# Kernel tuning notes

Measured on AMD Instinct MI355X. Metric: run time of the kernel, lower is better.

The kernel has to match this reference:

```python
import jax, jax.numpy as jnp
import numpy as np

N_NODES = 100000
N_EDGES = 2500000
N_GRAPHS = 1024


def setup_inputs() -> dict:
    key = jax.random.key(0)
    ks = jax.random.split(key, 12)
    inp = {
        "x": jax.random.normal(ks[0], (N_NODES, 7), dtype=jnp.float32),
        "e": jax.random.uniform(ks[1], (N_EDGES,), dtype=jnp.float32),
        "W1": jax.random.normal(ks[2], (7, 32), dtype=jnp.float32) * 0.3,
        "b1": jnp.zeros((32,), dtype=jnp.float32),
        "W2": jax.random.normal(ks[3], (32, 32), dtype=jnp.float32) * 0.2,
        "b2": jnp.zeros((32,), dtype=jnp.float32),
        "W3": jax.random.normal(ks[4], (32, 32), dtype=jnp.float32) * 0.2,
        "b3": jnp.zeros((32,), dtype=jnp.float32),
        "W4": jax.random.normal(ks[5], (32, 2), dtype=jnp.float32) * 0.2,
        "b4": jnp.zeros((2,), dtype=jnp.float32),
        "src": jax.random.randint(ks[6], (N_EDGES,), 0, N_NODES, dtype=jnp.int32),
        "dst": jax.random.randint(ks[7], (N_EDGES,), 0, N_NODES, dtype=jnp.int32),
        "graph_id": jnp.sort(jax.random.randint(ks[8], (N_NODES,), 0, N_GRAPHS, dtype=jnp.int32)),
        "n_graphs": N_GRAPHS,
    }
    return inp


def _graph_conv(feat, W, b, src, dst, norm_out, norm_in, edge_weight=None):
    # DGL GraphConv, norm='both': D_out^{-1/2} -> (weighted) sum aggregation -> D_in^{-1/2} -> linear
    n = feat.shape[0]
    h = feat * norm_out[:, None]
    m = h[src]  # [E, d] gather
    if edge_weight is not None:
        m = m * edge_weight[:, None]
    agg = jax.ops.segment_sum(m, dst, num_segments=n)  # [N, d]
    agg = agg * norm_in[:, None]
    return agg @ W + b


def reference(x, e, W1, b1, W2, b2, W3, b3, W4, b4, src, dst, graph_id, n_graphs):
    n = x.shape[0]
    ones_e = jnp.ones((src.shape[0],), dtype=x.dtype)
    deg_out = jax.ops.segment_sum(ones_e, src, num_segments=n)
    deg_in = jax.ops.segment_sum(ones_e, dst, num_segments=n)
    norm_out = jax.lax.rsqrt(jnp.clip(deg_out, 1.0))  # degs.clamp(min=1)^{-1/2}
    norm_in = jax.lax.rsqrt(jnp.clip(deg_in, 1.0))

    h = jax.nn.relu(_graph_conv(x, W1, b1, src, dst, norm_out, norm_in, edge_weight=e))
    h = jax.nn.relu(_graph_conv(h, W2, b2, src, dst, norm_out, norm_in))
    h = jax.nn.relu(_graph_conv(h, W3, b3, src, dst, norm_out, norm_in))
    h = _graph_conv(h, W4, b4, src, dst, norm_out, norm_in)

    # dgl.mean_nodes: per-graph mean of node features
    sums = jax.ops.segment_sum(h, graph_id, num_segments=n_graphs)  # [G, 2]
    cnts = jax.ops.segment_sum(jnp.ones((n,), dtype=h.dtype), graph_id, num_segments=n_graphs)
    return sums / jnp.clip(cnts, 1.0)[:, None]
```

## Files before the change

### kernel.cpp

```cpp
#include <hip/hip_runtime.h>

#define NN 100000
#define NE 2500000
#define BK_SHIFT 7
#define BK_NODES 128
#define NBUCK ((NN + BK_NODES - 1) / BK_NODES)
#define TILE 4096
#define NTILES ((NE + TILE - 1) / TILE)
#define SRC_MASK 0x1FFFF


__global__ __launch_bounds__(256) void k_tilecnt2(const int* __restrict__ src,
                                                  const int* __restrict__ dst,
                                                  int* __restrict__ tot_d, int* __restrict__ tot_s,
                                                  int E) {
    __shared__ int cd[NBUCK];
    __shared__ int cs[NBUCK];
    int base = blockIdx.x * TILE;
    for (int i = threadIdx.x; i < NBUCK; i += 256) { cd[i] = 0; cs[i] = 0; }
    __syncthreads();
#pragma unroll
    for (int k = 0; k < 16; ++k) {
        int idx = base + threadIdx.x + k * 256;
        if (idx < E) {
            atomicAdd(&cd[dst[idx] >> BK_SHIFT], 1);
            atomicAdd(&cs[src[idx] >> BK_SHIFT], 1);
        }
    }
    __syncthreads();
    for (int i = threadIdx.x; i < NBUCK; i += 256) {
        int c = cd[i]; if (c) atomicAdd(&tot_d[i], c);
        c = cs[i];     if (c) atomicAdd(&tot_s[i], c);
    }
}

__global__ __launch_bounds__(1024) void k_bucket_scan(const int* __restrict__ tot_d,
                                                      const int* __restrict__ tot_s,
                                                      int* __restrict__ base_d, int* __restrict__ base_s,
                                                      int* __restrict__ cursor_d, int* __restrict__ cursor_s,
                                                      int* __restrict__ row_ptr, int E) {
    __shared__ int sh[1024];
    int tid = threadIdx.x;
    int v = (tid < NBUCK) ? tot_d[tid] : 0;
    sh[tid] = v;
    __syncthreads();
#pragma unroll
    for (int off = 1; off < 1024; off <<= 1) {
        int t = (tid >= off) ? sh[tid - off] : 0;
        __syncthreads();
        sh[tid] += t;
        __syncthreads();
    }
    if (tid < NBUCK) { int ex = sh[tid] - v; base_d[tid] = ex; cursor_d[tid] = ex; }
    if (tid == 0) { base_d[NBUCK] = E; row_ptr[NN] = E; }
    __syncthreads();
    v = (tid < NBUCK) ? tot_s[tid] : 0;
    sh[tid] = v;
    __syncthreads();
#pragma unroll
    for (int off = 1; off < 1024; off <<= 1) {
        int t = (tid >= off) ? sh[tid - off] : 0;
        __syncthreads();
        sh[tid] += t;
        __syncthreads();
    }
    if (tid < NBUCK) { int ex = sh[tid] - v; base_s[tid] = ex; cursor_s[tid] = ex; }
    if (tid == 0) base_s[NBUCK] = E;
}

__global__ __launch_bounds__(256) void k_binpass2(
    const int* __restrict__ src, const int* __restrict__ dst, const float* __restrict__ ew,
    int* __restrict__ cursor_d, int* __restrict__ cursor_s,
    int2* __restrict__ stage2, unsigned char* __restrict__ stage_s, int E) {
    __shared__ int cnt_d[NBUCK];
    __shared__ int gpos_d[NBUCK];
    __shared__ int cnt_s[NBUCK];
    __shared__ int gpos_s[NBUCK];

    int base = blockIdx.x * TILE;
    for (int i = threadIdx.x; i < NBUCK; i += 256) { cnt_d[i] = 0; cnt_s[i] = 0; }
    __syncthreads();

    int w0[16]; float w1[16]; int pd[16]; int rs[16];
#pragma unroll
    for (int k = 0; k < 16; ++k) {
        int idx = base + threadIdx.x + k * 256;
        pd[k] = -1;
        if (idx < E) {
            int s = src[idx], d = dst[idx];
            w1[k] = ew[idx];
            int bd = d >> BK_SHIFT;
            w0[k] = s | ((d & (BK_NODES - 1)) << 17);
            int rd = atomicAdd(&cnt_d[bd], 1);
            pd[k] = bd | (rd << 10);
            rs[k] = atomicAdd(&cnt_s[s >> BK_SHIFT], 1);
        }
    }
    __syncthreads();

    for (int i = threadIdx.x; i < NBUCK; i += 256) {
        int c = cnt_d[i]; if (c) gpos_d[i] = atomicAdd(&cursor_d[i], c);
        c = cnt_s[i];     if (c) gpos_s[i] = atomicAdd(&cursor_s[i], c);
    }
    __syncthreads();

#pragma unroll
    for (int k = 0; k < 16; ++k) {
        if (pd[k] >= 0) {
            int bd = pd[k] & 1023, rd = pd[k] >> 10;
            stage2[gpos_d[bd] + rd] = make_int2(w0[k], __float_as_int(w1[k]));
            int s = w0[k] & SRC_MASK;
            stage_s[gpos_s[s >> BK_SHIFT] + rs[k]] = (unsigned char)(s & (BK_NODES - 1));
        }
    }
}

__global__ __launch_bounds__(256) void k_prep_src(
    const int* __restrict__ base_s, const unsigned char* __restrict__ stage_s, const float* __restrict__ x,
    float* __restrict__ no, float* __restrict__ xs, int N) {
    __shared__ int cnt[BK_NODES];
    int b = blockIdx.x;
    int beg = base_s[b], end = base_s[b + 1];
    if (threadIdx.x < BK_NODES) cnt[threadIdx.x] = 0;
    __syncthreads();
    for (int j = beg + threadIdx.x; j < end; j += 256) atomicAdd(&cnt[stage_s[j]], 1);
    __syncthreads();
    if (threadIdx.x < BK_NODES) {
        int n = (b << BK_SHIFT) + threadIdx.x;
        if (n < N) {
            float nov = rsqrtf(fmaxf((float)cnt[threadIdx.x], 1.0f));
            no[n] = nov;
#pragma unroll
            for (int f = 0; f < 7; ++f) xs[n * 8 + f] = x[n * 7 + f] * nov;
            xs[n * 8 + 7] = 0.f;
        }
    }
}

__global__ __launch_bounds__(256) void k_scatter2(
    const int* __restrict__ base_d, const int2* __restrict__ stage2,
    int* __restrict__ row_ptr, float* __restrict__ ni,
    int* __restrict__ csr_src, float* __restrict__ csr_w, int N) {
    __shared__ int cnt[BK_NODES];
    __shared__ int scn[BK_NODES];
    __shared__ int cur[BK_NODES];
    int b = blockIdx.x;
    int beg = base_d[b], end = base_d[b + 1];
    if (threadIdx.x < BK_NODES) cnt[threadIdx.x] = 0;
    __syncthreads();
    for (int j = beg + threadIdx.x; j < end; j += 256) atomicAdd(&cnt[stage2[j].x >> 17], 1);
    __syncthreads();
    int v = (threadIdx.x < BK_NODES) ? cnt[threadIdx.x] : 0;
    if (threadIdx.x < BK_NODES) scn[threadIdx.x] = v;
    __syncthreads();
#pragma unroll
    for (int off = 1; off < BK_NODES; off <<= 1) {
        int t = (threadIdx.x < BK_NODES && threadIdx.x >= off) ? scn[threadIdx.x - off] : 0;
        __syncthreads();
        if (threadIdx.x < BK_NODES) scn[threadIdx.x] += t;
        __syncthreads();
    }
    if (threadIdx.x < BK_NODES) {
        int ex = scn[threadIdx.x] - v;
        cur[threadIdx.x] = beg + ex;
        int n = (b << BK_SHIFT) + threadIdx.x;
        if (n < N) {
            row_ptr[n] = beg + ex;
            ni[n] = rsqrtf(fmaxf((float)v, 1.0f));
        }
    }
    __syncthreads();
    for (int j = beg + threadIdx.x; j < end; j += 256) {
        int2 t = stage2[j];
        int dl = t.x >> 17;
        int pos = atomicAdd(&cur[dl], 1);
        csr_src[pos] = t.x & SRC_MASK;
        csr_w[pos] = __int_as_float(t.y);
    }
}


__global__ __launch_bounds__(256) void k_layer1(
    const int* __restrict__ rp, const int* __restrict__ csr_src, const float* __restrict__ csr_w,
    const float* __restrict__ xs, const float* __restrict__ ni, const float* __restrict__ no,
    const float* __restrict__ W1, const float* __restrict__ b1, float* __restrict__ h1c, int N) {
    __shared__ float sW[7 * 32];
    __shared__ float sb[32];
    __shared__ float sh7[32][8];
    for (int i = threadIdx.x; i < 7 * 32; i += 256) sW[i] = W1[i];
    if (threadIdx.x < 32) sb[threadIdx.x] = b1[threadIdx.x];

    int g = threadIdx.x >> 3, lane = threadIdx.x & 7;
    int node = blockIdx.x * 32 + g;
    float acc = 0.f;
    if (node < N) {
        int beg = rp[node], end = rp[node + 1];
        for (int j0 = beg; j0 < end; j0 += 8) {
            int ms = 0; float mw = 0.f;
            if (j0 + lane < end) {
                ms = csr_src[j0 + lane];
                mw = csr_w[j0 + lane];
            }
            int m = end - j0; if (m > 8) m = 8;
            float a0 = 0.f, a1 = 0.f, a2 = 0.f, a3 = 0.f;
            int k = 0;
            for (; k + 4 <= m; k += 4) {
                int s0 = __shfl(ms, k, 8);     float w0 = __shfl(mw, k, 8);
                int s1 = __shfl(ms, k + 1, 8); float w1 = __shfl(mw, k + 1, 8);
                int s2 = __shfl(ms, k + 2, 8); float w2 = __shfl(mw, k + 2, 8);
                int s3 = __shfl(ms, k + 3, 8); float w3 = __shfl(mw, k + 3, 8);
                a0 += xs[s0 * 8 + lane] * w0;
                a1 += xs[s1 * 8 + lane] * w1;
                a2 += xs[s2 * 8 + lane] * w2;
                a3 += xs[s3 * 8 + lane] * w3;
            }
            for (; k < m; ++k) {
                int s = __shfl(ms, k, 8);
                float w = __shfl(mw, k, 8);
                a0 += xs[s * 8 + lane] * w;
            }
            acc += (a0 + a1) + (a2 + a3);
        }
        acc *= ni[node];
    }
    sh7[g][lane] = acc;
    __syncthreads();

    int g2 = threadIdx.x >> 5, l32 = threadIdx.x & 31;
#pragma unroll
    for (int t = 0; t < 4; ++t) {
        int nl = t * 8 + g2;
        int node2 = blockIdx.x * 32 + nl;
        if (node2 < N) {
            float o = sb[l32];
#pragma unroll
            for (int k = 0; k < 7; ++k) o += sh7[nl][k] * sW[k * 32 + l32];
            h1c[(size_t)(l32 >> 3) * N * 8 + (size_t)node2 * 8 + (l32 & 7)] =
                fmaxf(o, 0.f) * no[node2];
        }
    }
}

__device__ __forceinline__ void proc8(int msr, int mm, const float* __restrict__ tbl, int lane,
                                      float& a0, float& a1, float& a2, float& a3) {
    if (mm >= 8) {
        a0 += tbl[__shfl(msr, 0, 8) * 8 + lane];
        a1 += tbl[__shfl(msr, 1, 8) * 8 + lane];
        a2 += tbl[__shfl(msr, 2, 8) * 8 + lane];
        a3 += tbl[__shfl(msr, 3, 8) * 8 + lane];
        a0 += tbl[__shfl(msr, 4, 8) * 8 + lane];
        a1 += tbl[__shfl(msr, 5, 8) * 8 + lane];
        a2 += tbl[__shfl(msr, 6, 8) * 8 + lane];
        a3 += tbl[__shfl(msr, 7, 8) * 8 + lane];
    } else {
        int kl = 0;
        for (; kl + 4 <= mm; kl += 4) {
            a0 += tbl[__shfl(msr, kl, 8) * 8 + lane];
            a1 += tbl[__shfl(msr, kl + 1, 8) * 8 + lane];
            a2 += tbl[__shfl(msr, kl + 2, 8) * 8 + lane];
            a3 += tbl[__shfl(msr, kl + 3, 8) * 8 + lane];
        }
        for (; kl < mm; ++kl) a0 += tbl[__shfl(msr, kl, 8) * 8 + lane];
    }
}

__global__ __launch_bounds__(256) void k_aggc(
    const int* __restrict__ rp, const int* __restrict__ csr_src, const float* __restrict__ hc_in,
    const float* __restrict__ ni, float* __restrict__ aggout, int N) {
    int g = threadIdx.x >> 3, lane = threadIdx.x & 7;
    int c = blockIdx.y;
    int node = blockIdx.x * 32 + g;
    if (node >= N) return;
    const float* tbl = hc_in + (size_t)c * N * 8;
    int beg = rp[node], end = rp[node + 1];
    float acc = 0.f;
    for (int j0 = beg; j0 < end; j0 += 32) {
        int m = end - j0; if (m > 32) m = 32;
        int ms0 = (j0 + lane < end) ? csr_src[j0 + lane] : 0;
        int ms1 = (j0 + 8 + lane < end) ? csr_src[j0 + 8 + lane] : 0;
        int ms2 = (j0 + 16 + lane < end) ? csr_src[j0 + 16 + lane] : 0;
        int ms3 = (j0 + 24 + lane < end) ? csr_src[j0 + 24 + lane] : 0;
        float a0 = 0.f, a1 = 0.f, a2 = 0.f, a3 = 0.f;
        proc8(ms0, m, tbl, lane, a0, a1, a2, a3);
        if (m > 8)  proc8(ms1, m - 8, tbl, lane, a0, a1, a2, a3);
        if (m > 16) proc8(ms2, m - 16, tbl, lane, a0, a1, a2, a3);
        if (m > 24) proc8(ms3, m - 24, tbl, lane, a0, a1, a2, a3);
        acc += (a0 + a1) + (a2 + a3);
    }
    acc *= ni[node];
    aggout[(size_t)c * N * 8 + (size_t)node * 8 + lane] = acc;
}

__global__ __launch_bounds__(256) void k_mm2(
    const float* __restrict__ agg, const float* __restrict__ W, const float* __restrict__ bia,
    const float* __restrict__ no, float* __restrict__ hc_out, int N) {
    __shared__ float sW[32 * 32];
    __shared__ float sb[32];
    __shared__ float shv[8][32];
    for (int i = threadIdx.x; i < 1024; i += 256) sW[i] = W[i];
    if (threadIdx.x < 32) sb[threadIdx.x] = bia[threadIdx.x];
    int g = threadIdx.x >> 5, lane = threadIdx.x & 31;
    int n = blockIdx.x * 8 + g;
    if (n < N)
        shv[g][lane] = agg[(size_t)(lane >> 3) * N * 8 + (size_t)n * 8 + (lane & 7)];
    __syncthreads();
    if (n < N) {
        float o = sb[lane];
#pragma unroll
        for (int k = 0; k < 32; ++k) o += shv[g][k] * sW[k * 32 + lane];
        hc_out[(size_t)(lane >> 3) * N * 8 + (size_t)n * 8 + (lane & 7)] =
            fmaxf(o, 0.f) * no[n];
    }
}

__global__ __launch_bounds__(256) void k_mm3(
    const float* __restrict__ agg, const float* __restrict__ W3, const float* __restrict__ b3,
    const float* __restrict__ W4, const float* __restrict__ no, float2* __restrict__ h4pre, int N) {
    __shared__ float sW[32 * 32];
    __shared__ float sb[32];
    __shared__ float sW4[64];
    __shared__ float shv[8][32];
    for (int i = threadIdx.x; i < 1024; i += 256) sW[i] = W3[i];
    if (threadIdx.x < 32) sb[threadIdx.x] = b3[threadIdx.x];
    if (threadIdx.x < 64) sW4[threadIdx.x] = W4[threadIdx.x];
    int g = threadIdx.x >> 5, lane = threadIdx.x & 31;
    int n = blockIdx.x * 8 + g;
    if (n < N)
        shv[g][lane] = agg[(size_t)(lane >> 3) * N * 8 + (size_t)n * 8 + (lane & 7)];
    __syncthreads();
    if (n < N) {
        float o = sb[lane];
#pragma unroll
        for (int k = 0; k < 32; ++k) o += shv[g][k] * sW[k * 32 + lane];
        float t = fmaxf(o, 0.f) * no[n];
        float px = t * sW4[lane * 2 + 0];
        float py = t * sW4[lane * 2 + 1];
#pragma unroll
        for (int off = 16; off; off >>= 1) {
            px += __shfl_xor(px, off, 32);
            py += __shfl_xor(py, off, 32);
        }
        if (lane == 0) h4pre[n] = make_float2(px, py);
    }
}

__global__ void k_agg4(const int* __restrict__ rp, const int* __restrict__ csr_src,
                       const float2* __restrict__ h4pre, const float* __restrict__ ni,
                       float2* __restrict__ agg2, int N) {
    int n = blockIdx.x * blockDim.x + threadIdx.x;
    if (n >= N) return;
    int beg = rp[n], end = rp[n + 1];
    float ax0 = 0.f, ay0 = 0.f, ax1 = 0.f, ay1 = 0.f;
    int j = beg;
    for (; j + 2 <= end; j += 2) {
        int s0 = csr_src[j], s1 = csr_src[j + 1];
        float2 v0 = h4pre[s0];
        float2 v1 = h4pre[s1];
        ax0 += v0.x; ay0 += v0.y;
        ax1 += v1.x; ay1 += v1.y;
    }
    if (j < end) {
        float2 v = h4pre[csr_src[j]];
        ax0 += v.x; ay0 += v.y;
    }
    float w = ni[n];
    agg2[n] = make_float2((ax0 + ax1) * w, (ay0 + ay1) * w);
}

__global__ void k_pool(const float2* __restrict__ agg2, const int* __restrict__ gid,
                       const float* __restrict__ b4, float* __restrict__ out, int N) {
    int g = blockIdx.x;
    int lo = 0, hi = N;
    while (lo < hi) { int m = (lo + hi) >> 1; if (gid[m] < g) lo = m + 1; else hi = m; }
    int start = lo;
    int lo2 = start, hi2 = N;
    while (lo2 < hi2) { int m = (lo2 + hi2) >> 1; if (gid[m] < g + 1) lo2 = m + 1; else hi2 = m; }
    int end = lo2;
    float sx = 0.f, sy = 0.f;
    for (int n = start + threadIdx.x; n < end; n += 64) {
        float2 v = agg2[n];
        sx += v.x;
        sy += v.y;
    }
#pragma unroll
    for (int off = 32; off; off >>= 1) {
        sx += __shfl_down(sx, off, 64);
        sy += __shfl_down(sy, off, 64);
    }
    if (threadIdx.x == 0) {
        int cnt = end - start;
        float inv = 1.0f / fmaxf((float)cnt, 1.0f);
        float scale = (float)cnt * inv;
        out[g * 2 + 0] = sx * inv + b4[0] * scale;
        out[g * 2 + 1] = sy * inv + b4[1] * scale;
    }
}


extern "C" void kernel_launch(void* const* d_in, const int* in_sizes, int n_in,
                              void* d_out, int out_size, void* d_ws, size_t ws_size,
                              hipStream_t stream) {
    const float* x   = (const float*)d_in[0];
    const float* e   = (const float*)d_in[1];
    const float* W1  = (const float*)d_in[2];
    const float* b1  = (const float*)d_in[3];
    const float* W2  = (const float*)d_in[4];
    const float* b2  = (const float*)d_in[5];
    const float* W3  = (const float*)d_in[6];
    const float* b3  = (const float*)d_in[7];
    const float* W4  = (const float*)d_in[8];
    const float* b4  = (const float*)d_in[9];
    const int*   src = (const int*)d_in[10];
    const int*   dst = (const int*)d_in[11];
    const int*   gid = (const int*)d_in[12];
    float* out = (float*)d_out;

    const int N = NN, E = NE;
    const int G = out_size / 2;

    int* ws_i = (int*)d_ws;
    int* tot_d    = ws_i;
    int* tot_s    = ws_i + 1024;
    int* base_d   = ws_i + 2048;
    int* base_s   = ws_i + 3072;
    int* cursor_d = ws_i + 4096;
    int* cursor_s = ws_i + 5120;
    int* row_ptr  = ws_i + 6144;
    int* csr_src  = ws_i + 6144 + (size_t)N + 4;
    float* csr_w  = (float*)(ws_i + 6144 + (size_t)N + 4 + (size_t)E);
    unsigned char* stage_s = (unsigned char*)csr_w;

    float* fbase = (float*)(ws_i + 6144 + (size_t)N + 4 + 2 * (size_t)E);
    float* no_b  = fbase;
    float* ni_b  = fbase + (size_t)N;
    float* xs    = fbase + (size_t)2 * N;
    float* h1c   = fbase + (size_t)10 * N;
    float* h2c   = fbase + (size_t)42 * N;
    float2* h4pre = (float2*)(fbase + (size_t)74 * N);
    float2* agg2  = (float2*)(fbase + (size_t)76 * N);
    int2* stage2 = (int2*)(fbase + (size_t)10 * N);
    float* agg3 = h1c;

    hipMemsetAsync(ws_i, 0, 2048 * sizeof(int), stream);

    k_tilecnt2<<<NTILES, 256, 0, stream>>>(src, dst, tot_d, tot_s, E);
    k_bucket_scan<<<1, 1024, 0, stream>>>(tot_d, tot_s, base_d, base_s, cursor_d, cursor_s, row_ptr, E);
    k_binpass2<<<NTILES, 256, 0, stream>>>(src, dst, e, cursor_d, cursor_s, stage2, stage_s, E);
    k_prep_src<<<NBUCK, 256, 0, stream>>>(base_s, stage_s, x, no_b, xs, N);
    k_scatter2<<<NBUCK, 256, 0, stream>>>(base_d, stage2, row_ptr, ni_b, csr_src, csr_w, N);

    dim3 gAgg((N + 31) / 32, 4);
    k_layer1<<<(N + 31) / 32, 256, 0, stream>>>(row_ptr, csr_src, csr_w, xs, ni_b, no_b, W1, b1, h1c, N);
    k_aggc<<<gAgg, 256, 0, stream>>>(row_ptr, csr_src, h1c, ni_b, h2c, N);
    k_mm2<<<(N + 7) / 8, 256, 0, stream>>>(h2c, W2, b2, no_b, h2c, N);
    k_aggc<<<gAgg, 256, 0, stream>>>(row_ptr, csr_src, h2c, ni_b, agg3, N);
    k_mm3<<<(N + 7) / 8, 256, 0, stream>>>(agg3, W3, b3, W4, no_b, h4pre, N);
    k_agg4<<<(N + 255) / 256, 256, 0, stream>>>(row_ptr, csr_src, h4pre, ni_b, agg2, N);
    k_pool<<<G, 64, 0, stream>>>(agg2, gid, b4, out, N);
}
```

Measured before the change: 469.9 us.

## Switch hidden features to row-major and aggregate full 32-wide rows per wave

Hidden activations move from four channel-chunked 8-float planes to a row-major [N,32] layout. The aggregation kernel now uses one 64-lane wave per node, with each 8-lane group fetching whole 128-byte rows as float4 and a shuffle reduction across groups. This replaces four separate grid passes over the CSR indices with a single pass and widens each gather. The cost is one wave per node, so low-degree nodes leave lanes idle, plus the cross-group reduction overhead.

New measurement: 461.8 us. Within noise of the previous version (-1.7%).

```diff
diff --git a/kernel.cpp b/kernel.cpp
--- a/kernel.cpp
+++ b/kernel.cpp
@@ -183,7 +183,7 @@
 __global__ __launch_bounds__(256) void k_layer1(
     const int* __restrict__ rp, const int* __restrict__ csr_src, const float* __restrict__ csr_w,
     const float* __restrict__ xs, const float* __restrict__ ni, const float* __restrict__ no,
-    const float* __restrict__ W1, const float* __restrict__ b1, float* __restrict__ h1c, int N) {
+    const float* __restrict__ W1, const float* __restrict__ b1, float* __restrict__ h1s, int N) {
     __shared__ float sW[7 * 32];
     __shared__ float sb[32];
     __shared__ float sh7[32][8];
@@ -235,65 +235,62 @@
             float o = sb[l32];
 #pragma unroll
             for (int k = 0; k < 7; ++k) o += sh7[nl][k] * sW[k * 32 + l32];
-            h1c[(size_t)(l32 >> 3) * N * 8 + (size_t)node2 * 8 + (l32 & 7)] =
-                fmaxf(o, 0.f) * no[node2];
-        }
-    }
-}
-
-__device__ __forceinline__ void proc8(int msr, int mm, const float* __restrict__ tbl, int lane,
-                                      float& a0, float& a1, float& a2, float& a3) {
-    if (mm >= 8) {
-        a0 += tbl[__shfl(msr, 0, 8) * 8 + lane];
-        a1 += tbl[__shfl(msr, 1, 8) * 8 + lane];
-        a2 += tbl[__shfl(msr, 2, 8) * 8 + lane];
-        a3 += tbl[__shfl(msr, 3, 8) * 8 + lane];
-        a0 += tbl[__shfl(msr, 4, 8) * 8 + lane];
-        a1 += tbl[__shfl(msr, 5, 8) * 8 + lane];
-        a2 += tbl[__shfl(msr, 6, 8) * 8 + lane];
-        a3 += tbl[__shfl(msr, 7, 8) * 8 + lane];
-    } else {
-        int kl = 0;
-        for (; kl + 4 <= mm; kl += 4) {
-            a0 += tbl[__shfl(msr, kl, 8) * 8 + lane];
-            a1 += tbl[__shfl(msr, kl + 1, 8) * 8 + lane];
-            a2 += tbl[__shfl(msr, kl + 2, 8) * 8 + lane];
-            a3 += tbl[__shfl(msr, kl + 3, 8) * 8 + lane];
-        }
-        for (; kl < mm; ++kl) a0 += tbl[__shfl(msr, kl, 8) * 8 + lane];
-    }
-}
-
-__global__ __launch_bounds__(256) void k_aggc(
-    const int* __restrict__ rp, const int* __restrict__ csr_src, const float* __restrict__ hc_in,
+            h1s[(size_t)node2 * 32 + l32] = fmaxf(o, 0.f) * no[node2];
+        }
+    }
+}
+
+__global__ __launch_bounds__(256) void k_aggF(
+    const int* __restrict__ rp, const int* __restrict__ csr_src, const float* __restrict__ h_in,
     const float* __restrict__ ni, float* __restrict__ aggout, int N) {
-    int g = threadIdx.x >> 3, lane = threadIdx.x & 7;
-    int c = blockIdx.y;
-    int node = blockIdx.x * 32 + g;
+    int wave = threadIdx.x >> 6;
+    int lane = threadIdx.x & 63;
+    int g = lane >> 3, sub = lane & 7;
+    int node = blockIdx.x * 4 + wave;
     if (node >= N) return;
-    const float* tbl = hc_in + (size_t)c * N * 8;
     int beg = rp[node], end = rp[node + 1];
-    float acc = 0.f;
-    for (int j0 = beg; j0 < end; j0 += 32) {
-        int m = end - j0; if (m > 32) m = 32;
-        int ms0 = (j0 + lane < end) ? csr_src[j0 + lane] : 0;
-        int ms1 = (j0 + 8 + lane < end) ? csr_src[j0 + 8 + lane] : 0;
-        int ms2 = (j0 + 16 + lane < end) ? csr_src[j0 + 16 + lane] : 0;
-        int ms3 = (j0 + 24 + lane < end) ? csr_src[j0 + 24 + lane] : 0;
-        float a0 = 0.f, a1 = 0.f, a2 = 0.f, a3 = 0.f;
-        proc8(ms0, m, tbl, lane, a0, a1, a2, a3);
-        if (m > 8)  proc8(ms1, m - 8, tbl, lane, a0, a1, a2, a3);
-        if (m > 16) proc8(ms2, m - 16, tbl, lane, a0, a1, a2, a3);
-        if (m > 24) proc8(ms3, m - 24, tbl, lane, a0, a1, a2, a3);
-        acc += (a0 + a1) + (a2 + a3);
-    }
-    acc *= ni[node];
-    aggout[(size_t)c * N * 8 + (size_t)node * 8 + lane] = acc;
+
+    float4 A0 = make_float4(0.f, 0.f, 0.f, 0.f);
+    float4 A1 = A0, A2 = A0, A3 = A0;
+    int last = end - 1;
+
+    for (int j0 = beg + g; j0 < end; j0 += 32) {
+        int i1 = j0 + 8, i2 = j0 + 16, i3 = j0 + 24;
+        int s0 = csr_src[j0];
+        int s1 = csr_src[i1 <= last ? i1 : last];
+        int s2 = csr_src[i2 <= last ? i2 : last];
+        int s3 = csr_src[i3 <= last ? i3 : last];
+        float4 v0 = *reinterpret_cast<const float4*>(&h_in[(size_t)s0 * 32 + sub * 4]);
+        float4 v1 = *reinterpret_cast<const float4*>(&h_in[(size_t)s1 * 32 + sub * 4]);
+        float4 v2 = *reinterpret_cast<const float4*>(&h_in[(size_t)s2 * 32 + sub * 4]);
+        float4 v3 = *reinterpret_cast<const float4*>(&h_in[(size_t)s3 * 32 + sub * 4]);
+        A0.x += v0.x; A0.y += v0.y; A0.z += v0.z; A0.w += v0.w;
+        if (i1 < end) { A1.x += v1.x; A1.y += v1.y; A1.z += v1.z; A1.w += v1.w; }
+        if (i2 < end) { A2.x += v2.x; A2.y += v2.y; A2.z += v2.z; A2.w += v2.w; }
+        if (i3 < end) { A3.x += v3.x; A3.y += v3.y; A3.z += v3.z; A3.w += v3.w; }
+    }
+
+    float ax = (A0.x + A1.x) + (A2.x + A3.x);
+    float ay = (A0.y + A1.y) + (A2.y + A3.y);
+    float az = (A0.z + A1.z) + (A2.z + A3.z);
+    float aw = (A0.w + A1.w) + (A2.w + A3.w);
+#pragma unroll
+    for (int off = 8; off <= 32; off <<= 1) {
+        ax += __shfl_xor(ax, off, 64);
+        ay += __shfl_xor(ay, off, 64);
+        az += __shfl_xor(az, off, 64);
+        aw += __shfl_xor(aw, off, 64);
+    }
+    if (g == 0) {
+        float w = ni[node];
+        float4 o = make_float4(ax * w, ay * w, az * w, aw * w);
+        *reinterpret_cast<float4*>(&aggout[(size_t)node * 32 + sub * 4]) = o;
+    }
 }
 
 __global__ __launch_bounds__(256) void k_mm2(
     const float* __restrict__ agg, const float* __restrict__ W, const float* __restrict__ bia,
-    const float* __restrict__ no, float* __restrict__ hc_out, int N) {
+    const float* __restrict__ no, float* __restrict__ h_out, int N) {
     __shared__ float sW[32 * 32];
     __shared__ float sb[32];
     __shared__ float shv[8][32];
@@ -301,15 +298,13 @@
     if (threadIdx.x < 32) sb[threadIdx.x] = bia[threadIdx.x];
     int g = threadIdx.x >> 5, lane = threadIdx.x & 31;
     int n = blockIdx.x * 8 + g;
-    if (n < N)
-        shv[g][lane] = agg[(size_t)(lane >> 3) * N * 8 + (size_t)n * 8 + (lane & 7)];
+    if (n < N) shv[g][lane] = agg[(size_t)n * 32 + lane];
     __syncthreads();
     if (n < N) {
         float o = sb[lane];
 #pragma unroll
         for (int k = 0; k < 32; ++k) o += shv[g][k] * sW[k * 32 + lane];
-        hc_out[(size_t)(lane >> 3) * N * 8 + (size_t)n * 8 + (lane & 7)] =
-            fmaxf(o, 0.f) * no[n];
+        h_out[(size_t)n * 32 + lane] = fmaxf(o, 0.f) * no[n];
     }
 }
 
@@ -325,8 +320,7 @@
     if (threadIdx.x < 64) sW4[threadIdx.x] = W4[threadIdx.x];
     int g = threadIdx.x >> 5, lane = threadIdx.x & 31;
     int n = blockIdx.x * 8 + g;
-    if (n < N)
-        shv[g][lane] = agg[(size_t)(lane >> 3) * N * 8 + (size_t)n * 8 + (lane & 7)];
+    if (n < N) shv[g][lane] = agg[(size_t)n * 32 + lane];
     __syncthreads();
     if (n < N) {
         float o = sb[lane];
@@ -434,12 +428,12 @@
     float* no_b  = fbase;
     float* ni_b  = fbase + (size_t)N;
     float* xs    = fbase + (size_t)2 * N;
-    float* h1c   = fbase + (size_t)10 * N;
-    float* h2c   = fbase + (size_t)42 * N;
+    float* h1    = fbase + (size_t)10 * N;
+    float* h2    = fbase + (size_t)42 * N;
     float2* h4pre = (float2*)(fbase + (size_t)74 * N);
     float2* agg2  = (float2*)(fbase + (size_t)76 * N);
     int2* stage2 = (int2*)(fbase + (size_t)10 * N);
-    float* agg3 = h1c;
+    float* agg3 = h1;
 
     hipMemsetAsync(ws_i, 0, 2048 * sizeof(int), stream);
 
@@ -449,11 +443,10 @@
     k_prep_src<<<NBUCK, 256, 0, stream>>>(base_s, stage_s, x, no_b, xs, N);
     k_scatter2<<<NBUCK, 256, 0, stream>>>(base_d, stage2, row_ptr, ni_b, csr_src, csr_w, N);
 
-    dim3 gAgg((N + 31) / 32, 4);
-    k_layer1<<<(N + 31) / 32, 256, 0, stream>>>(row_ptr, csr_src, csr_w, xs, ni_b, no_b, W1, b1, h1c, N);
-    k_aggc<<<gAgg, 256, 0, stream>>>(row_ptr, csr_src, h1c, ni_b, h2c, N);
-    k_mm2<<<(N + 7) / 8, 256, 0, stream>>>(h2c, W2, b2, no_b, h2c, N);
-    k_aggc<<<gAgg, 256, 0, stream>>>(row_ptr, csr_src, h2c, ni_b, agg3, N);
+    k_layer1<<<(N + 31) / 32, 256, 0, stream>>>(row_ptr, csr_src, csr_w, xs, ni_b, no_b, W1, b1, h1, N);
+    k_aggF<<<(N + 3) / 4, 256, 0, stream>>>(row_ptr, csr_src, h1, ni_b, h2, N);
+    k_mm2<<<(N + 7) / 8, 256, 0, stream>>>(h2, W2, b2, no_b, h2, N);
+    k_aggF<<<(N + 3) / 4, 256, 0, stream>>>(row_ptr, csr_src, h2, ni_b, agg3, N);
     k_mm3<<<(N + 7) / 8, 256, 0, stream>>>(agg3, W3, b3, W4, no_b, h4pre, N);
     k_agg4<<<(N + 255) / 256, 256, 0, stream>>>(row_ptr, csr_src, h4pre, ni_b, agg2, N);
     k_pool<<<G, 64, 0, stream>>>(agg2, gid, b4, out, N);
```
